# Optimization experiments

Hardware: AMD Instinct MI355X
Metric: run time of the kernel (lower is better)

Reference implementation:

```python
import jax, jax.numpy as jnp
import numpy as np

N_NODES = 50000


def _gcn_conv(x, W, b, src, dst, n):
    """PyG GCNConv: add self-loops, symmetric normalization, sum-aggregate."""
    h = x @ W  # [N, out_dim] dense transform first (out_dim <= in_dim path)
    loop = jnp.arange(n, dtype=src.dtype)
    src_sl = jnp.concatenate([src, loop])
    dst_sl = jnp.concatenate([dst, loop])
    # degree computed on destination nodes (incl. self-loops)
    deg = jax.ops.segment_sum(jnp.ones_like(dst_sl, dtype=h.dtype), dst_sl, num_segments=n)
    dinv = jnp.where(deg > 0, jax.lax.rsqrt(deg), 0.0)
    norm = dinv[src_sl] * dinv[dst_sl]  # [E+N]
    msgs = h[src_sl] * norm[:, None]  # gather + scale, [E+N, out_dim]
    out = jax.ops.segment_sum(msgs, dst_sl, num_segments=n)  # scatter-add
    return out + b


def setup_inputs() -> dict:
    key = jax.random.key(0)
    k0, k1, k2, k3 = jax.random.split(key, 4)
    d = 256
    E = 400000
    scale = 1.0 / np.sqrt(d)
    x = jax.random.normal(k0, (N_NODES, d), dtype=jnp.float32)
    edge_index = jax.random.randint(k1, (2, E), 0, N_NODES, dtype=jnp.int64)
    W1 = jax.random.normal(k2, (d, d), dtype=jnp.float32) * scale
    b1 = jnp.zeros((d,), dtype=jnp.float32)
    W2 = jax.random.normal(k3, (d, d), dtype=jnp.float32) * scale
    b2 = jnp.zeros((d,), dtype=jnp.float32)
    return {"x": x, "edge_index": edge_index, "W1": W1, "b1": b1, "W2": W2, "b2": b2}


def reference(x, edge_index, W1, b1, W2, b2):
    src, dst = edge_index[0], edge_index[1]
    h = _gcn_conv(x, W1, b1, src, dst, N_NODES)
    h = jax.nn.relu(h)
    h = _gcn_conv(h, W2, b2, src, dst, N_NODES)
    h = jax.nn.relu(h)
    return h
```

## Files before the change

kernel.cpp:

```cpp
#include <hip/hip_runtime.h>
#include <stdint.h>

typedef __bf16 bf16_t;
typedef bf16_t bf16x4 __attribute__((ext_vector_type(4)));
typedef bf16_t bf16x8 __attribute__((ext_vector_type(8)));
typedef float f32x4 __attribute__((ext_vector_type(4)));

#define DIM 256
#define NNODES 50000

__device__ __forceinline__ int detect_f64(const int* __restrict__ ei) {
    int v = ei[2 * (threadIdx.x & 63) + 1];
    unsigned long long m = __ballot(v == 0);
    return __popcll(m) > 32;
}

__device__ __forceinline__ int load_edge(const int* __restrict__ ei, int E, int f64,
                                         int which , int e) {
    int v = f64 ? ei[(size_t)which * 2 * E + 2 * (size_t)e]
                : ei[(size_t)which * E + (size_t)e];
    return min(max(v, 0), NNODES - 1);
}


__global__ void hist_kernel(const int* __restrict__ ei, int E, int* __restrict__ counts) {
    int f64 = detect_f64(ei);
    int e = blockIdx.x * blockDim.x + threadIdx.x;
    if (e < E) atomicAdd(&counts[load_edge(ei, E, f64, 1, e)], 1);
}

__global__ __launch_bounds__(256) void scanA_kernel(const int* __restrict__ counts,
                                                    int* __restrict__ offsets,
                                                    int* __restrict__ bsums, int n) {
    __shared__ int sm[256];
    int b = blockIdx.x, t = threadIdx.x;
    int idx = b * 256 + t;
    int v = (idx < n) ? counts[idx] : 0;
    sm[t] = v;
    __syncthreads();
    #pragma unroll
    for (int off = 1; off < 256; off <<= 1) {
        int u = (t >= off) ? sm[t - off] : 0;
        __syncthreads();
        sm[t] += u;
        __syncthreads();
    }
    if (idx < n) offsets[idx + 1] = sm[t];
    if (t == 255) bsums[b] = sm[255];
}

__global__ __launch_bounds__(256) void scanB_kernel(int* __restrict__ bsums, int nb) {
    __shared__ int sm[256];
    int t = threadIdx.x;
    int v = (t < nb) ? bsums[t] : 0;
    sm[t] = v;
    __syncthreads();
    #pragma unroll
    for (int off = 1; off < 256; off <<= 1) {
        int u = (t >= off) ? sm[t - off] : 0;
        __syncthreads();
        sm[t] += u;
        __syncthreads();
    }
    if (t < nb) bsums[t] = sm[t] - v;
}

__global__ __launch_bounds__(256) void scanC_kernel(const int* __restrict__ counts,
                                                    const int* __restrict__ bsums,
                                                    int* __restrict__ offsets,
                                                    float* __restrict__ dinv,
                                                    int* __restrict__ cursor, int n) {
    int b = blockIdx.x;
    int idx = b * 256 + threadIdx.x;
    if (idx == 0) offsets[0] = 0;
    if (idx < n) {
        int incl = offsets[idx + 1] + bsums[b];
        offsets[idx + 1] = incl;
        cursor[idx] = incl - counts[idx];
        dinv[idx] = rsqrtf((float)(counts[idx] + 1));
    }
}

__global__ void scatter_kernel(const int* __restrict__ ei, int E,
                               const float* __restrict__ dinv, int* __restrict__ cursor,
                               int2* __restrict__ csr_e) {
    int f64 = detect_f64(ei);
    int e = blockIdx.x * blockDim.x + threadIdx.x;
    if (e < E) {
        int s = load_edge(ei, E, f64, 0, e);
        int d = load_edge(ei, E, f64, 1, e);
        int pos = atomicAdd(&cursor[d], 1);
        if (pos >= 0 && pos < E) {
            int2 v;
            v.x = s;
            v.y = __float_as_int(dinv[s] * dinv[d]);
            csr_e[pos] = v;
        }
    }
}


__global__ void convert_w_kernel(const float* __restrict__ W1, const float* __restrict__ W2,
                                 bf16_t* __restrict__ Wf1, bf16_t* __restrict__ Wf2) {
    const float* W = blockIdx.y ? W2 : W1;
    bf16_t* Wf = blockIdx.y ? Wf2 : Wf1;
    int k = blockIdx.x, n = threadIdx.x;
    int s = k >> 5, quad = (k >> 3) & 3, j = k & 7;
    int nt = n >> 4, m = n & 15;
    Wf[s * 8192 + (nt * 64 + quad * 16 + m) * 8 + j] = (bf16_t)W[k * DIM + n];
}


template <bool F32A>
__global__ __launch_bounds__(256, 4) void gemm_kernel(const void* __restrict__ Xv,
                                                      const bf16_t* __restrict__ Wf,
                                                      bf16_t* __restrict__ H, int tiles) {
    __shared__ bf16_t sB[8192];
    int tid = threadIdx.x;
    int wave = tid >> 6, lane = tid & 63;
    int m = lane & 15, quad = lane >> 4;
    int tile = blockIdx.x * 4 + wave;
    bool active = tile < tiles;
    int arow = (min(tile, tiles - 1)) * 16 + m;

    f32x4 acc[16] = {};

    for (int s = 0; s < 8; s++) {
        __syncthreads();
        {
            const bf16x8* g = (const bf16x8*)Wf + s * 1024;
            bf16x8* d = (bf16x8*)sB;
            #pragma unroll
            for (int it = 0; it < 4; it++) d[tid + it * 256] = g[tid + it * 256];
        }
        __syncthreads();

        bf16x8 a;
        if (F32A) {
            const f32x4* xp = (const f32x4*)((const float*)Xv + (size_t)arow * DIM + s * 32 + quad * 8);
            f32x4 x0 = xp[0], x1 = xp[1];
            #pragma unroll
            for (int j = 0; j < 4; j++) { a[j] = (bf16_t)x0[j]; a[j + 4] = (bf16_t)x1[j]; }
        } else {
            a = *(const bf16x8*)((const bf16_t*)Xv + (size_t)arow * DIM + s * 32 + quad * 8);
        }

        #pragma unroll
        for (int nt = 0; nt < 16; nt++) {
            bf16x8 b = *(const bf16x8*)(sB + nt * 512 + lane * 8);
            acc[nt] = __builtin_amdgcn_mfma_f32_16x16x32_bf16(a, b, acc[nt], 0, 0, 0);
        }
    }

    if (active) {
        int rowb = tile * 16 + quad * 4;
        #pragma unroll
        for (int nt = 0; nt < 16; nt++) {
            #pragma unroll
            for (int r = 0; r < 4; r++) {
                H[(size_t)(rowb + r) * DIM + nt * 16 + m] = (bf16_t)acc[nt][r];
            }
        }
    }
}


template <int OUT_BF16>
__global__ __launch_bounds__(256) void aggregate_kernel(const bf16_t* __restrict__ H,
                                                        const int* __restrict__ offsets,
                                                        const int2* __restrict__ csr_e,
                                                        const float* __restrict__ dinv,
                                                        const float* __restrict__ bias,
                                                        void* __restrict__ outv, int n) {
    int wg = threadIdx.x >> 5;
    int l = threadIdx.x & 31;
    int i = blockIdx.x * 8 + wg;
    if (i >= n) return;

    const char* Hb = (const char*)H;
    int doff = l * 16;

    auto cvt = [](bf16x4 v) -> f32x4 {
        f32x4 r;
        #pragma unroll
        for (int j = 0; j < 4; j++) r[j] = (float)v[j];
        return r;
    };
    auto lo4 = [](bf16x8 v) -> bf16x4 { return __builtin_shufflevector(v, v, 0, 1, 2, 3); };
    auto hi4 = [](bf16x8 v) -> bf16x4 { return __builtin_shufflevector(v, v, 4, 5, 6, 7); };

    float dii = dinv[i];
    bf16x8 selfv = *(const bf16x8*)(Hb + ((size_t)i << 9) + doff);
    f32x4 acc0 = cvt(lo4(selfv)) * (dii * dii);
    f32x4 acc1 = cvt(hi4(selfv)) * (dii * dii);

    int e0 = offsets[i], e1 = offsets[i + 1];
    int e = e0;
    for (; e + 8 <= e1; e += 8) {
        unsigned s[8]; float w[8];
        #pragma unroll
        for (int j = 0; j < 8; j++) {
            int2 t = csr_e[e + j];
            s[j] = min((unsigned)t.x, (unsigned)(NNODES - 1));
            w[j] = __int_as_float(t.y);
        }
        bf16x8 h[8];
        #pragma unroll
        for (int j = 0; j < 8; j++) {
            h[j] = *(const bf16x8*)(Hb + ((size_t)s[j] << 9) + doff);
        }
        __builtin_amdgcn_sched_barrier(0);
        #pragma unroll
        for (int j = 0; j < 8; j++) {
            acc0 += cvt(lo4(h[j])) * w[j];
            acc1 += cvt(hi4(h[j])) * w[j];
        }
    }
    if (e < e1) {
        unsigned s[8]; float w[8];
        #pragma unroll
        for (int j = 0; j < 8; j++) {
            bool valid = (e + j) < e1;
            int2 t = csr_e[valid ? e + j : e];
            if (!valid) { t.x = i; t.y = 0; }
            s[j] = min((unsigned)t.x, (unsigned)(NNODES - 1));
            w[j] = __int_as_float(t.y);
        }
        bf16x8 h[8];
        #pragma unroll
        for (int j = 0; j < 8; j++) {
            h[j] = *(const bf16x8*)(Hb + ((size_t)s[j] << 9) + doff);
        }
        __builtin_amdgcn_sched_barrier(0);
        #pragma unroll
        for (int j = 0; j < 8; j++) {
            acc0 += cvt(lo4(h[j])) * w[j];
            acc1 += cvt(hi4(h[j])) * w[j];
        }
    }

    const f32x4* bp = (const f32x4*)(bias + l * 8);
    acc0 += bp[0];
    acc1 += bp[1];
    #pragma unroll
    for (int j = 0; j < 4; j++) {
        acc0[j] = fmaxf(acc0[j], 0.0f);
        acc1[j] = fmaxf(acc1[j], 0.0f);
    }

    if (OUT_BF16) {
        bf16x8 o;
        #pragma unroll
        for (int j = 0; j < 4; j++) { o[j] = (bf16_t)acc0[j]; o[j + 4] = (bf16_t)acc1[j]; }
        *(bf16x8*)((bf16_t*)outv + (size_t)i * DIM + l * 8) = o;
    } else {
        float* op = (float*)outv + (size_t)i * DIM + l * 8;
        *(f32x4*)op = acc0;
        *(f32x4*)(op + 4) = acc1;
    }
}


extern "C" void kernel_launch(void* const* d_in, const int* in_sizes, int n_in,
                              void* d_out, int out_size, void* d_ws, size_t ws_size,
                              hipStream_t stream) {
    const float* x  = (const float*)d_in[0];
    const int*   ei = (const int*)d_in[1];
    const float* W1 = (const float*)d_in[2];
    const float* b1 = (const float*)d_in[3];
    const float* W2 = (const float*)d_in[4];
    const float* b2 = (const float*)d_in[5];
    float* out = (float*)d_out;

    const int n = NNODES;
    const int E = in_sizes[1] / 2;
    const int nb = (n + 255) / 256;

    char* ws = (char*)d_ws;
    size_t off = 0;
    auto alloc = [&](size_t bytes) -> char* {
        char* p = ws + off;
        off += (bytes + 255) & ~(size_t)255;
        return p;
    };
    float*  dinv     = (float*)alloc((size_t)n * 4);
    int*    counts   = (int*)alloc((size_t)n * 4);
    int*    offsets  = (int*)alloc((size_t)(n + 1) * 4);
    int*    cursor   = (int*)alloc((size_t)n * 4);
    int*    bsums    = (int*)alloc((size_t)nb * 4);
    int2*   csr_e    = (int2*)alloc((size_t)E * 8);
    bf16_t* Wf1      = (bf16_t*)alloc((size_t)DIM * DIM * 2);
    bf16_t* Wf2      = (bf16_t*)alloc((size_t)DIM * DIM * 2);
    bf16_t* P        = (bf16_t*)alloc((size_t)n * DIM * 2);
    bf16_t* X2       = (bf16_t*)alloc((size_t)n * DIM * 2);

    hipMemsetAsync(counts, 0, (size_t)n * 4, stream);
    hist_kernel<<<(E + 255) / 256, 256, 0, stream>>>(ei, E, counts);
    scanA_kernel<<<nb, 256, 0, stream>>>(counts, offsets, bsums, n);
    scanB_kernel<<<1, 256, 0, stream>>>(bsums, nb);
    scanC_kernel<<<nb, 256, 0, stream>>>(counts, bsums, offsets, dinv, cursor, n);
    scatter_kernel<<<(E + 255) / 256, 256, 0, stream>>>(ei, E, dinv, cursor, csr_e);

    convert_w_kernel<<<dim3(DIM, 2), DIM, 0, stream>>>(W1, W2, Wf1, Wf2);

    int tiles = (n + 15) / 16;
    int gemm_blocks = (tiles + 3) / 4;
    int agg_blocks = (n + 7) / 8;

    gemm_kernel<true><<<gemm_blocks, 256, 0, stream>>>(x, Wf1, P, tiles);
    aggregate_kernel<1><<<agg_blocks, 256, 0, stream>>>(P, offsets, csr_e, dinv, b1, X2, n);
    gemm_kernel<false><<<gemm_blocks, 256, 0, stream>>>(X2, Wf2, P, tiles);
    aggregate_kernel<0><<<agg_blocks, 256, 0, stream>>>(P, offsets, csr_e, dinv, b2, out, n);
}
```

Before: 258.2 us.

## Fuse preprocessing launches: merge memset+weight convert, gemm1+histogram, single-pass scan

The counts memset and the weight conversion now run in one prep kernel. The degree histogram runs as extra blocks inside the first GEMM launch so the two overlap, and the three-kernel scan becomes one kernel where each block recomputes its prefix base by summing the earlier counts. The aim is to cut kernel launch count and inter-kernel gaps in the short preprocessing phase. The cost is redundant reads in the scan (later blocks sum up to 50K counts each) and histogram atomics competing with GEMM blocks.

```diff
diff --git a/kernel.cpp b/kernel.cpp
--- a/kernel.cpp
+++ b/kernel.cpp
@@ -23,17 +23,111 @@
 }
 
 
-__global__ void hist_kernel(const int* __restrict__ ei, int E, int* __restrict__ counts) {
-    int f64 = detect_f64(ei);
-    int e = blockIdx.x * blockDim.x + threadIdx.x;
-    if (e < E) atomicAdd(&counts[load_edge(ei, E, f64, 1, e)], 1);
-}
-
-__global__ __launch_bounds__(256) void scanA_kernel(const int* __restrict__ counts,
-                                                    int* __restrict__ offsets,
-                                                    int* __restrict__ bsums, int n) {
+__global__ __launch_bounds__(256) void prep_kernel(int* __restrict__ counts,
+                                                   const float* __restrict__ W1,
+                                                   const float* __restrict__ W2,
+                                                   bf16_t* __restrict__ Wf1,
+                                                   bf16_t* __restrict__ Wf2, int n) {
+    const int nb = (NNODES + 255) / 256;
+    int b = blockIdx.x, t = threadIdx.x;
+    if (b < nb) {
+        int idx = b * 256 + t;
+        if (idx < n) counts[idx] = 0;
+    } else {
+        int cw = b - nb;
+        const float* W = (cw & 256) ? W2 : W1;
+        bf16_t* Wf = (cw & 256) ? Wf2 : Wf1;
+        int k = cw & 255;
+        int s = k >> 5, quad = (k >> 3) & 3, j = k & 7;
+        int nt = t >> 4, m = t & 15;
+        Wf[s * 8192 + (nt * 64 + quad * 16 + m) * 8 + j] = (bf16_t)W[k * DIM + t];
+    }
+}
+
+
+__global__ __launch_bounds__(256, 4) void gemm1_hist_kernel(const float* __restrict__ X,
+                                                            const bf16_t* __restrict__ Wf,
+                                                            bf16_t* __restrict__ H, int tiles,
+                                                            int gemm_blocks,
+                                                            const int* __restrict__ ei, int E,
+                                                            int* __restrict__ counts) {
+    __shared__ bf16_t sB[8192];
+    if ((int)blockIdx.x >= gemm_blocks) {
+        int f64 = detect_f64(ei);
+        int e = (blockIdx.x - gemm_blocks) * 256 + threadIdx.x;
+        if (e < E) atomicAdd(&counts[load_edge(ei, E, f64, 1, e)], 1);
+        return;
+    }
+
+    int tid = threadIdx.x;
+    int wave = tid >> 6, lane = tid & 63;
+    int m = lane & 15, quad = lane >> 4;
+    int tile = blockIdx.x * 4 + wave;
+    bool active = tile < tiles;
+    int arow = (min(tile, tiles - 1)) * 16 + m;
+
+    f32x4 acc[16] = {};
+
+    for (int s = 0; s < 8; s++) {
+        __syncthreads();
+        {
+            const bf16x8* g = (const bf16x8*)Wf + s * 1024;
+            bf16x8* d = (bf16x8*)sB;
+            #pragma unroll
+            for (int it = 0; it < 4; it++) d[tid + it * 256] = g[tid + it * 256];
+        }
+        __syncthreads();
+
+        bf16x8 a;
+        const f32x4* xp = (const f32x4*)(X + (size_t)arow * DIM + s * 32 + quad * 8);
+        f32x4 x0 = xp[0], x1 = xp[1];
+        #pragma unroll
+        for (int j = 0; j < 4; j++) { a[j] = (bf16_t)x0[j]; a[j + 4] = (bf16_t)x1[j]; }
+
+        #pragma unroll
+        for (int nt = 0; nt < 16; nt++) {
+            bf16x8 b = *(const bf16x8*)(sB + nt * 512 + lane * 8);
+            acc[nt] = __builtin_amdgcn_mfma_f32_16x16x32_bf16(a, b, acc[nt], 0, 0, 0);
+        }
+    }
+
+    if (active) {
+        int rowb = tile * 16 + quad * 4;
+        #pragma unroll
+        for (int nt = 0; nt < 16; nt++) {
+            #pragma unroll
+            for (int r = 0; r < 4; r++) {
+                H[(size_t)(rowb + r) * DIM + nt * 16 + m] = (bf16_t)acc[nt][r];
+            }
+        }
+    }
+}
+
+
+__global__ __launch_bounds__(256) void scan_kernel(const int* __restrict__ counts,
+                                                   int* __restrict__ offsets,
+                                                   int* __restrict__ cursor,
+                                                   float* __restrict__ dinv, int n) {
+    __shared__ int red[256];
     __shared__ int sm[256];
     int b = blockIdx.x, t = threadIdx.x;
+
+    int part = 0;
+    const int4* c4 = (const int4*)counts;
+    int lim = b * 64;
+    for (int j = t; j < lim; j += 256) {
+        int4 v = c4[j];
+        part += v.x + v.y + v.z + v.w;
+    }
+    red[t] = part;
+    __syncthreads();
+    #pragma unroll
+    for (int off = 128; off > 0; off >>= 1) {
+        if (t < off) red[t] += red[t + off];
+        __syncthreads();
+    }
+    int base = red[0];
+
     int idx = b * 256 + t;
     int v = (idx < n) ? counts[idx] : 0;
     sm[t] = v;
@@ -45,40 +139,13 @@
         sm[t] += u;
         __syncthreads();
     }
-    if (idx < n) offsets[idx + 1] = sm[t];
-    if (t == 255) bsums[b] = sm[255];
-}
-
-__global__ __launch_bounds__(256) void scanB_kernel(int* __restrict__ bsums, int nb) {
-    __shared__ int sm[256];
-    int t = threadIdx.x;
-    int v = (t < nb) ? bsums[t] : 0;
-    sm[t] = v;
-    __syncthreads();
-    #pragma unroll
-    for (int off = 1; off < 256; off <<= 1) {
-        int u = (t >= off) ? sm[t - off] : 0;
-        __syncthreads();
-        sm[t] += u;
-        __syncthreads();
-    }
-    if (t < nb) bsums[t] = sm[t] - v;
-}
-
-__global__ __launch_bounds__(256) void scanC_kernel(const int* __restrict__ counts,
-                                                    const int* __restrict__ bsums,
-                                                    int* __restrict__ offsets,
-                                                    float* __restrict__ dinv,
-                                                    int* __restrict__ cursor, int n) {
-    int b = blockIdx.x;
-    int idx = b * 256 + threadIdx.x;
+    if (idx < n) {
+        int incl = base + sm[t];
+        offsets[idx + 1] = incl;
+        cursor[idx] = incl - v;
+        dinv[idx] = rsqrtf((float)(v + 1));
+    }
     if (idx == 0) offsets[0] = 0;
-    if (idx < n) {
-        int incl = offsets[idx + 1] + bsums[b];
-        offsets[idx + 1] = incl;
-        cursor[idx] = incl - counts[idx];
-        dinv[idx] = rsqrtf((float)(counts[idx] + 1));
-    }
 }
 
 __global__ void scatter_kernel(const int* __restrict__ ei, int E,
@@ -100,19 +167,7 @@
 }
 
 
-__global__ void convert_w_kernel(const float* __restrict__ W1, const float* __restrict__ W2,
-                                 bf16_t* __restrict__ Wf1, bf16_t* __restrict__ Wf2) {
-    const float* W = blockIdx.y ? W2 : W1;
-    bf16_t* Wf = blockIdx.y ? Wf2 : Wf1;
-    int k = blockIdx.x, n = threadIdx.x;
-    int s = k >> 5, quad = (k >> 3) & 3, j = k & 7;
-    int nt = n >> 4, m = n & 15;
-    Wf[s * 8192 + (nt * 64 + quad * 16 + m) * 8 + j] = (bf16_t)W[k * DIM + n];
-}
-
-
-template <bool F32A>
-__global__ __launch_bounds__(256, 4) void gemm_kernel(const void* __restrict__ Xv,
+__global__ __launch_bounds__(256, 4) void gemm_kernel(const bf16_t* __restrict__ Xv,
                                                       const bf16_t* __restrict__ Wf,
                                                       bf16_t* __restrict__ H, int tiles) {
     __shared__ bf16_t sB[8192];
@@ -135,15 +190,7 @@
         }
         __syncthreads();
 
-        bf16x8 a;
-        if (F32A) {
-            const f32x4* xp = (const f32x4*)((const float*)Xv + (size_t)arow * DIM + s * 32 + quad * 8);
-            f32x4 x0 = xp[0], x1 = xp[1];
-            #pragma unroll
-            for (int j = 0; j < 4; j++) { a[j] = (bf16_t)x0[j]; a[j + 4] = (bf16_t)x1[j]; }
-        } else {
-            a = *(const bf16x8*)((const bf16_t*)Xv + (size_t)arow * DIM + s * 32 + quad * 8);
-        }
+        bf16x8 a = *(const bf16x8*)(Xv + (size_t)arow * DIM + s * 32 + quad * 8);
 
         #pragma unroll
         for (int nt = 0; nt < 16; nt++) {
@@ -287,28 +334,23 @@
     int*    counts   = (int*)alloc((size_t)n * 4);
     int*    offsets  = (int*)alloc((size_t)(n + 1) * 4);
     int*    cursor   = (int*)alloc((size_t)n * 4);
-    int*    bsums    = (int*)alloc((size_t)nb * 4);
     int2*   csr_e    = (int2*)alloc((size_t)E * 8);
     bf16_t* Wf1      = (bf16_t*)alloc((size_t)DIM * DIM * 2);
     bf16_t* Wf2      = (bf16_t*)alloc((size_t)DIM * DIM * 2);
     bf16_t* P        = (bf16_t*)alloc((size_t)n * DIM * 2);
     bf16_t* X2       = (bf16_t*)alloc((size_t)n * DIM * 2);
 
-    hipMemsetAsync(counts, 0, (size_t)n * 4, stream);
-    hist_kernel<<<(E + 255) / 256, 256, 0, stream>>>(ei, E, counts);
-    scanA_kernel<<<nb, 256, 0, stream>>>(counts, offsets, bsums, n);
-    scanB_kernel<<<1, 256, 0, stream>>>(bsums, nb);
-    scanC_kernel<<<nb, 256, 0, stream>>>(counts, bsums, offsets, dinv, cursor, n);
-    scatter_kernel<<<(E + 255) / 256, 256, 0, stream>>>(ei, E, dinv, cursor, csr_e);
-
-    convert_w_kernel<<<dim3(DIM, 2), DIM, 0, stream>>>(W1, W2, Wf1, Wf2);
-
     int tiles = (n + 15) / 16;
     int gemm_blocks = (tiles + 3) / 4;
+    int hist_blocks = (E + 255) / 256;
     int agg_blocks = (n + 7) / 8;
 
-    gemm_kernel<true><<<gemm_blocks, 256, 0, stream>>>(x, Wf1, P, tiles);
+    prep_kernel<<<nb + 512, 256, 0, stream>>>(counts, W1, W2, Wf1, Wf2, n);
+    gemm1_hist_kernel<<<gemm_blocks + hist_blocks, 256, 0, stream>>>(x, Wf1, P, tiles,
+                                                                     gemm_blocks, ei, E, counts);
+    scan_kernel<<<nb, 256, 0, stream>>>(counts, offsets, cursor, dinv, n);
+    scatter_kernel<<<hist_blocks, 256, 0, stream>>>(ei, E, dinv, cursor, csr_e);
     aggregate_kernel<1><<<agg_blocks, 256, 0, stream>>>(P, offsets, csr_e, dinv, b1, X2, n);
-    gemm_kernel<false><<<gemm_blocks, 256, 0, stream>>>(X2, Wf2, P, tiles);
+    gemm_kernel<<<gemm_blocks, 256, 0, stream>>>(X2, Wf2, P, tiles);
     aggregate_kernel<0><<<agg_blocks, 256, 0, stream>>>(P, offsets, csr_e, dinv, b2, out, n);
 }
```

Result: faster. 252.0 us (-2.4%).
